# Performance work log

Hardware: AMD Instinct MI355X
Metric: run time of the kernel (lower is better)

The kernel has to match this reference:

```python
import jax, jax.numpy as jnp
import numpy as np

N, E, DIN, DH, R = 50000, 1600000, 128, 128, 3


def setup_inputs() -> dict:
    key = jax.random.key(0)
    ks = jax.random.split(key, 32)
    inp = {}
    inp["x"] = jax.random.normal(ks[0], (N, DIN), jnp.float32)
    inp["h_prev"] = jax.random.normal(ks[1], (N, DH), jnp.float32)
    inp["edge_index"] = jax.random.randint(ks[2], (2, E), 0, N)
    inp["node_role"] = jax.random.randint(ks[3], (N,), 0, R)
    i = 4
    for name, din, has_b in (("xz", DIN, True), ("hz", DH, False), ("xr", DIN, True), ("hr", DH, False), ("xh", DIN, True), ("hh", DH, False)):
        inp[name + "_W"] = jax.random.normal(ks[i], (din, DH), jnp.float32) / np.float32(np.sqrt(din)); i += 1
        inp[name + "_Wg"] = jax.random.normal(ks[i], (R, DH), jnp.float32) * np.float32(0.1); i += 1
        inp[name + "_bg"] = jnp.zeros((R, DH), jnp.float32)
        inp[name + "_S"] = jax.random.normal(ks[i], (R, DH, DH), jnp.float32) / np.float32(np.sqrt(DH)); i += 1
        if has_b:
            inp[name + "_b"] = jnp.zeros((R, DH), jnp.float32)
    return inp


def _role_conv(x, W, Wg, bg, S, b, row, col, node_role):
    # x: [N, din] -> transformed features [N, DH]
    xt = x @ W
    r = node_role[row]                                  # role of source node per edge
    g = jax.nn.sigmoid(Wg[r] + bg[r])                   # [Etot, DH] role gate
    msg = xt[row] * g
    if b is not None:
        msg = msg + b[r]
    n = x.shape[0]
    summed = jax.ops.segment_sum(msg, col, num_segments=n)
    cnt = jax.ops.segment_sum(jnp.ones((row.shape[0],), xt.dtype), col, num_segments=n)
    aggr = summed / jnp.maximum(cnt, 1.0)[:, None]      # scatter_mean (self-loops ensure cnt>=1)
    # per-role self transform: out[i] = xt[i] @ S[role[i]] + aggr[i]
    out = aggr
    for nr in range(R):
        out = out + jnp.where((node_role == nr)[:, None], xt @ S[nr], jnp.float32(0.0))
    return jax.nn.relu(out)


def reference(x, edge_index, h_prev, node_role,
              xz_W, xz_Wg, xz_bg, xz_S, xz_b,
              hz_W, hz_Wg, hz_bg, hz_S,
              xr_W, xr_Wg, xr_bg, xr_S, xr_b,
              hr_W, hr_Wg, hr_bg, hr_S,
              xh_W, xh_Wg, xh_bg, xh_S, xh_b,
              hh_W, hh_Wg, hh_bg, hh_S):
    n = x.shape[0]
    loops = jnp.arange(n, dtype=edge_index.dtype)
    row = jnp.concatenate([edge_index[0], loops])       # add_self_loops appended at end
    col = jnp.concatenate([edge_index[1], loops])

    z = jax.nn.sigmoid(_role_conv(x, xz_W, xz_Wg, xz_bg, xz_S, xz_b, row, col, node_role)
                       + _role_conv(h_prev, hz_W, hz_Wg, hz_bg, hz_S, None, row, col, node_role))
    r = jax.nn.sigmoid(_role_conv(x, xr_W, xr_Wg, xr_bg, xr_S, xr_b, row, col, node_role)
                       + _role_conv(h_prev, hr_W, hr_Wg, hr_bg, hr_S, None, row, col, node_role))
    h_tilde = jnp.tanh(_role_conv(x, xh_W, xh_Wg, xh_bg, xh_S, xh_b, row, col, node_role)
                       + _role_conv(r * h_prev, hh_W, hh_Wg, hh_bg, hh_S, None, row, col, node_role))
    h_new = z * h_prev + (1.0 - z) * h_tilde
    return h_new
```

## Files before the change

### kernel.cpp

```cpp
#include <hip/hip_runtime.h>


typedef __bf16 bf16;
typedef __bf16 bf16x8 __attribute__((ext_vector_type(8)));
typedef float  f32x4  __attribute__((ext_vector_type(4)));
typedef float  f32x2  __attribute__((ext_vector_type(2)));
typedef unsigned char u8;

#define DH 128

__device__ __forceinline__ float sigmoidf_(float x) { return 1.0f / (1.0f + expf(-x)); }

__global__ __launch_bounds__(256) void hist_kernel(const int* __restrict__ ei, const int* __restrict__ role,
                                                   int* __restrict__ cnt3, int* __restrict__ rolecnt,
                                                   int E, int N)
{
  int i = blockIdx.x * 256 + threadIdx.x;
  int lane = threadIdx.x & 63;
  int r = (i < N) ? role[i] : -1;
  #pragma unroll
  for (int rr = 0; rr < 3; ++rr) {
    unsigned long long mask = __ballot(r == rr);
    if (lane == 0 && mask) atomicAdd(&rolecnt[rr], __popcll(mask));
  }
  if (i < E + N) {
    int src, dst;
    if (i < E) { src = ei[i]; dst = ei[E + i]; } else { src = i - E; dst = i - E; }
    int rs = (i < E) ? role[src] : r;
    if (i >= E) rs = role[i - E];
    atomicAdd(&cnt3[dst * 3 + rs], 1);
  }
}

__global__ __launch_bounds__(1024) void scan1_kernel(const int* __restrict__ cnt, int* __restrict__ off,
                                                     int* __restrict__ bsum, int n)
{
  __shared__ int wsum[16];
  int t = threadIdx.x, lane = t & 63, w = t >> 6;
  int idx = blockIdx.x * 1024 + t;
  int v = (idx < n) ? cnt[idx] : 0;
  int s = v;
  #pragma unroll
  for (int d = 1; d < 64; d <<= 1) { int u = __shfl_up(s, d); if (lane >= d) s += u; }
  if (lane == 63) wsum[w] = s;
  __syncthreads();
  if (w == 0 && lane < 16) {
    int ws = wsum[lane];
    #pragma unroll
    for (int d = 1; d < 16; d <<= 1) { int u = __shfl_up(ws, d); if (lane >= d) ws += u; }
    wsum[lane] = ws;
  }
  __syncthreads();
  int inc = ((w > 0) ? wsum[w - 1] : 0) + s;
  if (idx < n) off[idx + 1] = inc;
  if (t == 1023) bsum[blockIdx.x] = inc;
}

__global__ void scan2_kernel(int* __restrict__ bsum, int nb, const int* __restrict__ rolecnt,
                             int* __restrict__ rolefill, int* __restrict__ roleinfo)
{
  int lane = threadIdx.x;
  int carry = 0;
  for (int base = 0; base < nb; base += 64) {
    int v = (base + lane < nb) ? bsum[base + lane] : 0;
    int s = v;
    #pragma unroll
    for (int d = 1; d < 64; d <<= 1) { int u = __shfl_up(s, d); if (lane >= d) s += u; }
    if (base + lane < nb) bsum[base + lane] = carry + s - v;
    carry += __shfl(s, 63);
  }
  if (lane == 0) {
    int c0 = rolecnt[0], c1 = rolecnt[1], c2 = rolecnt[2];
    int s1 = (c0 + 255) & ~255;
    int s2 = s1 + ((c1 + 255) & ~255);
    int mp = s2 + ((c2 + 255) & ~255);
    rolefill[0] = 0; rolefill[1] = s1; rolefill[2] = s2;
    roleinfo[0] = s1; roleinfo[1] = s2;
    roleinfo[2] = c0;      roleinfo[3] = s1 - c0;
    roleinfo[4] = s1 + c1; roleinfo[5] = s2 - s1 - c1;
    roleinfo[6] = s2 + c2; roleinfo[7] = mp - s2 - c2;
  }
}

__global__ __launch_bounds__(1024) void scan3_kernel(int* __restrict__ off, int* __restrict__ fill,
                                                     const int* __restrict__ bsum, int n)
{
  int idx = blockIdx.x * 1024 + threadIdx.x;
  if (idx == 0) { off[0] = 0; fill[0] = 0; }
  if (idx < n) {
    int v = off[idx + 1] + bsum[blockIdx.x];
    off[idx + 1] = v;
    if (idx + 1 < n) fill[idx + 1] = v;
  }
}

__global__ void bucketinit_kernel(const int* __restrict__ off3, int* __restrict__ bucketfill,
                                  int NB, int W, int N)
{
  int b = blockIdx.x * 256 + threadIdx.x;
  if (b < NB) {
    int d = min(b * W, N);
    bucketfill[b] = off3[d * 3];
  }
}

__global__ __launch_bounds__(256) void partition_kernel(
    const int* __restrict__ ei, const int* __restrict__ spos,
    const int* __restrict__ roleinfo, int* __restrict__ bucketfill,
    int2* __restrict__ recs, int E, int N, int shiftB)
{
  __shared__ int lcnt[256], lbase[256];
  const int base = blockIdx.x * 4096;
  const int s1 = roleinfo[0], s2 = roleinfo[1];
  lcnt[threadIdx.x] = 0;
  __syncthreads();
  int myb[16], mybin[16], myt[16];
  #pragma unroll
  for (int k = 0; k < 16; ++k) {
    int i = base + k * 256 + threadIdx.x;
    myb[k] = -1;
    if (i < E + N) {
      int src, dst;
      if (i < E) { src = ei[i]; dst = ei[E + i]; } else { src = i - E; dst = i - E; }
      int t = spos[src];
      int r = (t >= s2) ? 2 : (t >= s1) ? 1 : 0;
      myb[k] = dst >> shiftB;
      mybin[k] = dst * 3 + r;
      myt[k] = t;
      atomicAdd(&lcnt[myb[k]], 1);
    }
  }
  __syncthreads();
  int c = lcnt[threadIdx.x];
  lbase[threadIdx.x] = (c > 0) ? atomicAdd(&bucketfill[threadIdx.x], c) : 0;
  __syncthreads();
  lcnt[threadIdx.x] = 0;
  __syncthreads();
  #pragma unroll
  for (int k = 0; k < 16; ++k) {
    if (myb[k] >= 0) {
      int slot = atomicAdd(&lcnt[myb[k]], 1);
      recs[lbase[myb[k]] + slot] = make_int2(mybin[k], myt[k]);
    }
  }
}

__global__ __launch_bounds__(1024) void binscatter_kernel(
    const int2* __restrict__ recs, const int* __restrict__ off3,
    int* __restrict__ fill3, int* __restrict__ ssrc, int W, int N)
{
  int b = blockIdx.x;
  int d0 = min(b * W, N), d1 = min((b + 1) * W, N);
  int s = off3[d0 * 3], e = off3[d1 * 3];
  for (int i = s + threadIdx.x; i < e; i += 1024) {
    int2 rec = recs[i];
    int pz = atomicAdd(&fill3[rec.x], 1);
    ssrc[pz] = rec.y;
  }
}

__global__ __launch_bounds__(256) void permscatter_kernel(const int* __restrict__ role, int* __restrict__ rolefill,
                                                          int* __restrict__ spos, int* __restrict__ sposinv, int N)
{
  int i = blockIdx.x * 256 + threadIdx.x;
  int lane = threadIdx.x & 63;
  int r = (i < N) ? role[i] : -1;
  #pragma unroll
  for (int rr = 0; rr < 3; ++rr) {
    unsigned long long mask = __ballot(r == rr);
    if (!mask) continue;
    int base = 0;
    if (lane == 0) base = atomicAdd(&rolefill[rr], __popcll(mask));
    base = __shfl(base, 0);
    if (r == rr) {
      int rank = (int)__popcll(mask & ((1ull << lane) - 1ull));
      int pos = base + rank;
      spos[i] = pos;
      sposinv[pos] = i;
    }
  }
}

__global__ __launch_bounds__(256) void zeropad_kernel(const int* __restrict__ roleinfo,
                                                      bf16* __restrict__ Ax, bf16* __restrict__ Ah)
{
  int id = blockIdx.x * 256 + threadIdx.x;
  int a = id / 49152, rem = id % 49152;
  int gp = rem / 16384, r2 = rem % 16384;
  int rr = r2 >> 6, c = r2 & 63;
  int gs = roleinfo[2 + gp * 2], gl = roleinfo[3 + gp * 2];
  if (rr < gl) {
    int row = gs + rr;
    size_t unit = (size_t)(row >> 4) * 1024 + c * 16 + (row & 15);
    bf16x8 z = {};
    ((bf16x8*)(a == 0 ? Ax : Ah))[unit] = z;
  }
}

__global__ __launch_bounds__(256) void prep_xh_kernel(const float* __restrict__ x, const float* __restrict__ h,
                                                      const int* __restrict__ spos, u8* __restrict__ xq8,
                                                      bf16* __restrict__ Ax, bf16* __restrict__ Ah, int N)
{
  int g = blockIdx.x * 256 + threadIdx.x;
  if (g >= N * 32) return;
  int n = g >> 5, j = g & 31;
  int t = spos[n];
  const float* src = (j < 16) ? (x + (size_t)n * 128 + (j << 3))
                              : (h + (size_t)n * 128 + ((j - 16) << 3));
  float4 v0 = ((const float4*)src)[0];
  float4 v1 = ((const float4*)src)[1];
  int lo = __builtin_amdgcn_cvt_pk_fp8_f32(v0.x, v0.y, 0, false);
  lo = __builtin_amdgcn_cvt_pk_fp8_f32(v0.z, v0.w, lo, true);
  int hi = __builtin_amdgcn_cvt_pk_fp8_f32(v1.x, v1.y, 0, false);
  hi = __builtin_amdgcn_cvt_pk_fp8_f32(v1.z, v1.w, hi, true);
  *(int2*)(xq8 + (size_t)t * 256 + j * 8) = make_int2(lo, hi);
  bf16x8 o;
  o[0] = (bf16)v0.x; o[1] = (bf16)v0.y; o[2] = (bf16)v0.z; o[3] = (bf16)v0.w;
  o[4] = (bf16)v1.x; o[5] = (bf16)v1.y; o[6] = (bf16)v1.z; o[7] = (bf16)v1.w;
  size_t unit = (size_t)(t >> 4) * 1024 + (48 + (j & 15)) * 16 + (t & 15);
  ((bf16x8*)(j < 16 ? Ax : Ah))[unit] = o;
}

struct PrepW { const float* W[6]; const float* Wg[6]; const float* bg[6]; };
__global__ __launch_bounds__(256) void prep_wf_kernel(PrepW pw, bf16* __restrict__ Wf)
{
  int idx = blockIdx.x * 256 + threadIdx.x;
  if (idx >= 294912) return;
  int cv = idx / 49152, pos = idx % 49152;
  int ks4q = pos >> 10;
  int col = (pos >> 3) & 127, j = pos & 7;
  int k = (ks4q >> 2) * 32 + (ks4q & 3) * 8 + j;
  int r = k >> 7, kk = k & 127;
  float g = sigmoidf_(pw.Wg[cv][r * 128 + col] + pw.bg[cv][r * 128 + col]);
  Wf[idx] = (bf16)(pw.W[cv][kk * 128 + col] * g);
}

struct PrepP { const float* W[6]; const float* S[6]; };
__global__ __launch_bounds__(128) void prep_pf_kernel(PrepP pp, bf16* __restrict__ Pf)
{
  int b = blockIdx.x;
  int cv = b / 384, rem = b % 384;
  int r = rem >> 7, kp = rem & 127;
  int col = threadIdx.x;
  const float* W = pp.W[cv] + (size_t)kp * 128;
  const float* S = pp.S[cv] + (size_t)r * 16384;
  float sum = 0.f;
  #pragma unroll 4
  for (int j2 = 0; j2 < 128; ++j2) sum += W[j2] * S[j2 * 128 + col];
  size_t o = (size_t)(cv * 3 + r) * 16384 + ((size_t)(kp >> 3) * 128 + col) * 8 + (kp & 7);
  Pf[o] = (bf16)sum;
}

#define ACCUM16(U, d) do { f32x2 f_;                                                   \
  f_ = __builtin_amdgcn_cvt_pk_f32_fp8((d).x, false); U[0]  += f_[0]; U[1]  += f_[1];  \
  f_ = __builtin_amdgcn_cvt_pk_f32_fp8((d).x, true);  U[2]  += f_[0]; U[3]  += f_[1];  \
  f_ = __builtin_amdgcn_cvt_pk_f32_fp8((d).y, false); U[4]  += f_[0]; U[5]  += f_[1];  \
  f_ = __builtin_amdgcn_cvt_pk_f32_fp8((d).y, true);  U[6]  += f_[0]; U[7]  += f_[1];  \
  f_ = __builtin_amdgcn_cvt_pk_f32_fp8((d).z, false); U[8]  += f_[0]; U[9]  += f_[1];  \
  f_ = __builtin_amdgcn_cvt_pk_f32_fp8((d).z, true);  U[10] += f_[0]; U[11] += f_[1];  \
  f_ = __builtin_amdgcn_cvt_pk_f32_fp8((d).w, false); U[12] += f_[0]; U[13] += f_[1];  \
  f_ = __builtin_amdgcn_cvt_pk_f32_fp8((d).w, true);  U[14] += f_[0]; U[15] += f_[1];  \
} while (0)

#define ACCSEL16(d, p) do {                      \
  if ((p) < o1)      { ACCUM16(u0, d); }         \
  else if ((p) < o2) { ACCUM16(u1, d); }         \
  else               { ACCUM16(u2, d); }         \
} while (0)

__global__ __launch_bounds__(512) void gather_xh_kernel(
    const u8* __restrict__ xq8, const int* __restrict__ off3, const int* __restrict__ ssrc,
    const int* __restrict__ sposinv, bf16* __restrict__ Ax, bf16* __restrict__ Ah,
    float4* __restrict__ cntf)
{
  __shared__ alignas(16) bf16 lds[8][768];
  int w = threadIdx.x >> 6, lane = threadIdx.x & 63;
  int t0 = blockIdx.x * 8;
  int t = t0 + w;
  int node = sposinv[t];
  int qt = lane >> 4, ql = lane & 15;

  if (node >= 0) {
    int o0 = __builtin_amdgcn_readfirstlane(off3[node * 3]);
    int o1 = __builtin_amdgcn_readfirstlane(off3[node * 3 + 1]);
    int o2 = __builtin_amdgcn_readfirstlane(off3[node * 3 + 2]);
    int o3 = __builtin_amdgcn_readfirstlane(off3[node * 3 + 3]);
    float inv = 1.0f / (float)(o3 - o0);
    const u8* base = xq8 + ql * 16;

    float u0[16], u1[16], u2[16];
    #pragma unroll
    for (int k = 0; k < 16; ++k) { u0[k] = 0.f; u1[k] = 0.f; u2[k] = 0.f; }

    const int e = o3, emax = o3 - 1;
    for (int i = o0; i < e; i += 16) {
      int p0 = i + qt, p1 = p0 + 4, p2 = p0 + 8, p3 = p0 + 12;
      int t0i = ssrc[min(p0, emax)];
      int t1i = ssrc[min(p1, emax)];
      int t2i = ssrc[min(p2, emax)];
      int t3i = ssrc[min(p3, emax)];
      int4 d0 = make_int4(0, 0, 0, 0), d1 = d0, d2 = d0, d3 = d0;
      if (p0 < e) d0 = *(const int4*)(base + (size_t)t0i * 256);
      if (p1 < e) d1 = *(const int4*)(base + (size_t)t1i * 256);
      if (p2 < e) d2 = *(const int4*)(base + (size_t)t2i * 256);
      if (p3 < e) d3 = *(const int4*)(base + (size_t)t3i * 256);
      ACCSEL16(d0, p0);
      ACCSEL16(d1, p1);
      ACCSEL16(d2, p2);
      ACCSEL16(d3, p3);
    }

    #pragma unroll
    for (int k = 0; k < 16; ++k) {
      u0[k] += __shfl_xor(u0[k], 16); u0[k] += __shfl_xor(u0[k], 32);
      u1[k] += __shfl_xor(u1[k], 16); u1[k] += __shfl_xor(u1[k], 32);
      u2[k] += __shfl_xor(u2[k], 16); u2[k] += __shfl_xor(u2[k], 32);
    }
    if (qt == 0) {
      bf16x8 p0v, p1v;
      int sb0 = (ql < 8) ? (ql * 16) : (384 + (ql - 8) * 16);
      #pragma unroll
      for (int k = 0; k < 8; ++k) { p0v[k] = (bf16)(u0[k] * inv); p1v[k] = (bf16)(u0[8 + k] * inv); }
      *(bf16x8*)&lds[w][sb0] = p0v;
      *(bf16x8*)&lds[w][sb0 + 8] = p1v;
      #pragma unroll
      for (int k = 0; k < 8; ++k) { p0v[k] = (bf16)(u1[k] * inv); p1v[k] = (bf16)(u1[8 + k] * inv); }
      *(bf16x8*)&lds[w][sb0 + 128] = p0v;
      *(bf16x8*)&lds[w][sb0 + 136] = p1v;
      #pragma unroll
      for (int k = 0; k < 8; ++k) { p0v[k] = (bf16)(u2[k] * inv); p1v[k] = (bf16)(u2[8 + k] * inv); }
      *(bf16x8*)&lds[w][sb0 + 256] = p0v;
      *(bf16x8*)&lds[w][sb0 + 264] = p1v;
    }
    if (lane == 0)
      cntf[t] = make_float4((o1 - o0) * inv, (o2 - o1) * inv, (o3 - o2) * inv, (float)(o3 - o0));
  } else {
    if (lane < 48) {
      bf16x8 z = {};
      *(bf16x8*)&lds[w][lane * 16] = z;
      *(bf16x8*)&lds[w][lane * 16 + 8] = z;
    }
    if (lane == 0) cntf[t] = make_float4(0.f, 0.f, 0.f, 0.f);
  }

  __syncthreads();

  int tid = threadIdx.x;
  if (tid < 384) {
    int lc = tid >> 3, row = tid & 7;
    size_t unit = (size_t)(t0 >> 4) * 1024 + lc * 16 + (t0 & 15) + row;
    __builtin_nontemporal_store(*(const bf16x8*)&lds[row][lc * 8], (bf16x8*)Ax + unit);
    __builtin_nontemporal_store(*(const bf16x8*)&lds[row][384 + lc * 8], (bf16x8*)Ah + unit);
  }
}

#define ACCUM8(U, d) do { f32x2 f_;                                                  \
  f_ = __builtin_amdgcn_cvt_pk_f32_fp8((d).x, false); U[0] += f_[0]; U[1] += f_[1];  \
  f_ = __builtin_amdgcn_cvt_pk_f32_fp8((d).x, true);  U[2] += f_[0]; U[3] += f_[1];  \
  f_ = __builtin_amdgcn_cvt_pk_f32_fp8((d).y, false); U[4] += f_[0]; U[5] += f_[1];  \
  f_ = __builtin_amdgcn_cvt_pk_f32_fp8((d).y, true);  U[6] += f_[0]; U[7] += f_[1];  \
} while (0)

#define ACCSEL8(d, p) do {                      \
  if ((p) < o1)      { ACCUM8(v0, d); }         \
  else if ((p) < o2) { ACCUM8(v1, d); }         \
  else               { ACCUM8(v2, d); }         \
} while (0)

__global__ __launch_bounds__(512) void gather_q_kernel(
    const u8* __restrict__ q8, const int* __restrict__ off3, const int* __restrict__ ssrc,
    const int* __restrict__ sposinv, bf16* __restrict__ Aq)
{
  __shared__ alignas(16) bf16 lds[8][384];
  int w = threadIdx.x >> 6, lane = threadIdx.x & 63;
  int t0 = blockIdx.x * 8;
  int t = t0 + w;
  int node = sposinv[t];
  int qt = lane >> 4, ql = lane & 15;

  if (node >= 0) {
    int o0 = __builtin_amdgcn_readfirstlane(off3[node * 3]);
    int o1 = __builtin_amdgcn_readfirstlane(off3[node * 3 + 1]);
    int o2 = __builtin_amdgcn_readfirstlane(off3[node * 3 + 2]);
    int o3 = __builtin_amdgcn_readfirstlane(off3[node * 3 + 3]);
    float inv = 1.0f / (float)(o3 - o0);
    const u8* base = q8 + ql * 8;

    float v0[8], v1[8], v2[8];
    #pragma unroll
    for (int k = 0; k < 8; ++k) { v0[k] = 0.f; v1[k] = 0.f; v2[k] = 0.f; }

    const int e = o3, emax = o3 - 1;
    for (int i = o0; i < e; i += 16) {
      int p0 = i + qt, p1 = p0 + 4, p2 = p0 + 8, p3 = p0 + 12;
      int t0i = ssrc[min(p0, emax)];
      int t1i = ssrc[min(p1, emax)];
      int t2i = ssrc[min(p2, emax)];
      int t3i = ssrc[min(p3, emax)];
      int2 d0 = make_int2(0, 0), d1 = d0, d2 = d0, d3 = d0;
      if (p0 < e) d0 = *(const int2*)(base + (size_t)t0i * 128);
      if (p1 < e) d1 = *(const int2*)(base + (size_t)t1i * 128);
      if (p2 < e) d2 = *(const int2*)(base + (size_t)t2i * 128);
      if (p3 < e) d3 = *(const int2*)(base + (size_t)t3i * 128);
      ACCSEL8(d0, p0);
      ACCSEL8(d1, p1);
      ACCSEL8(d2, p2);
      ACCSEL8(d3, p3);
    }

    #pragma unroll
    for (int k = 0; k < 8; ++k) {
      v0[k] += __shfl_xor(v0[k], 16); v0[k] += __shfl_xor(v0[k], 32);
      v1[k] += __shfl_xor(v1[k], 16); v1[k] += __shfl_xor(v1[k], 32);
      v2[k] += __shfl_xor(v2[k], 16); v2[k] += __shfl_xor(v2[k], 32);
    }
    if (qt == 0) {
      bf16x8 pk;
      #pragma unroll
      for (int k = 0; k < 8; ++k) pk[k] = (bf16)(v0[k] * inv);
      *(bf16x8*)&lds[w][ql * 8] = pk;
      #pragma unroll
      for (int k = 0; k < 8; ++k) pk[k] = (bf16)(v1[k] * inv);
      *(bf16x8*)&lds[w][128 + ql * 8] = pk;
      #pragma unroll
      for (int k = 0; k < 8; ++k) pk[k] = (bf16)(v2[k] * inv);
      *(bf16x8*)&lds[w][256 + ql * 8] = pk;
    }
  } else {
    if (lane < 48) {
      bf16x8 z = {};
      *(bf16x8*)&lds[w][lane * 8] = z;
    }
  }

  __syncthreads();

  int tid = threadIdx.x;
  if (tid < 384) {
    int lc = tid >> 3, row = tid & 7;
    size_t unit = (size_t)(t0 >> 4) * 1024 + lc * 16 + (t0 & 15) + row;
    __builtin_nontemporal_store(*(const bf16x8*)&lds[row][lc * 8], (bf16x8*)Aq + unit);
  }
}

struct GArgs {
  const bf16* Ap[5];
  const bf16* wf[5];
  const bf16* pf[5];
  bf16* out[5];
  const float* bias[5];
};

__global__ __launch_bounds__(256, 3) void gemm_kernel(GArgs ga, const float4* __restrict__ cntf,
                                                      const int* __restrict__ roleinfo)
{
  const int cv = blockIdx.y;
  const bf16* __restrict__ Ap = ga.Ap[cv];
  const bf16* __restrict__ wf = ga.wf[cv];
  const bf16* __restrict__ pf = ga.pf[cv];
  bf16* __restrict__ out = ga.out[cv];
  const float* __restrict__ bias = ga.bias[cv];

  const int w = threadIdx.x >> 6, lane = threadIdx.x & 63;
  const int q = lane >> 4, l = lane & 15;
  const int rb0 = blockIdx.x * 8 + w * 2;
  const int row0 = blockIdx.x * 128;
  const int s1 = roleinfo[0], s2 = roleinfo[1];
  const int role = (row0 >= s2) ? 2 : (row0 >= s1) ? 1 : 0;
  const int laneoff = q * 128 + l;

  f32x4 acc[2][8];
  #pragma unroll
  for (int j = 0; j < 2; ++j)
    #pragma unroll
    for (int ct = 0; ct < 8; ++ct)
      #pragma unroll
      for (int k = 0; k < 4; ++k) acc[j][ct][k] = 0.f;

  const bf16x8* A0 = (const bf16x8*)Ap + (size_t)rb0 * 1024 + lane;
  const bf16x8* WF = (const bf16x8*)wf + laneoff;
  const bf16x8* PF = (const bf16x8*)pf + role * 2048 + laneoff;

  #pragma unroll 2
  for (int ks = 0; ks < 16; ++ks) {
    const bf16x8* bp = (ks < 12) ? (WF + ks * 512) : (PF + (ks - 12) * 512);
    bf16x8 a0 = A0[ks * 64];
    bf16x8 a1 = A0[1024 + ks * 64];
    #pragma unroll
    for (int ct = 0; ct < 8; ++ct) {
      bf16x8 b = bp[ct * 16];
      acc[0][ct] = __builtin_amdgcn_mfma_f32_16x16x32_bf16(a0, b, acc[0][ct], 0, 0, 0);
      acc[1][ct] = __builtin_amdgcn_mfma_f32_16x16x32_bf16(a1, b, acc[1][ct], 0, 0, 0);
    }
  }

  const bool hb = (bias != nullptr);
  #pragma unroll
  for (int j = 0; j < 2; ++j) {
    int rb = rb0 + j;
    float4 cfs[4];
    if (hb) {
      #pragma unroll
      for (int reg = 0; reg < 4; ++reg) cfs[reg] = cntf[rb * 16 + q * 4 + reg];
    }
    #pragma unroll
    for (int ct = 0; ct < 8; ++ct) {
      int col = ct * 16 + l;
      float b0 = 0, b1 = 0, b2 = 0;
      if (hb) { b0 = bias[col]; b1 = bias[128 + col]; b2 = bias[256 + col]; }
      #pragma unroll
      for (int reg = 0; reg < 4; ++reg) {
        int t = rb * 16 + q * 4 + reg;
        float v = acc[j][ct][reg];
        if (hb) v += cfs[reg].x * b0 + cfs[reg].y * b1 + cfs[reg].z * b2;
        out[(size_t)t * 128 + col] = (bf16)fmaxf(v, 0.f);
      }
    }
  }
}

__global__ __launch_bounds__(256) void combine1_kernel(
    const bf16* __restrict__ o0, const bf16* __restrict__ o1,
    const bf16* __restrict__ o2, const bf16* __restrict__ o3,
    const float* __restrict__ h, const int* __restrict__ spos,
    float* __restrict__ zbuf, u8* __restrict__ q8, bf16* __restrict__ Aq, int N)
{
  int g = blockIdx.x * 256 + threadIdx.x;
  if (g >= N * 16) return;
  int n = g >> 4, o = g & 15;
  int t = spos[n];
  size_t tb = (size_t)t * 16 + o;
  bf16x8 a0 = ((const bf16x8*)o0)[tb];
  bf16x8 a1 = ((const bf16x8*)o1)[tb];
  bf16x8 a2 = ((const bf16x8*)o2)[tb];
  bf16x8 a3 = ((const bf16x8*)o3)[tb];
  size_t nb = (size_t)n * 16 + o;
  float4 h0 = ((const float4*)h)[nb * 2];
  float4 h1 = ((const float4*)h)[nb * 2 + 1];
  float hv[8] = {h0.x, h0.y, h0.z, h0.w, h1.x, h1.y, h1.z, h1.w};
  float zv[8], qv[8];
  bf16x8 qb;
  #pragma unroll
  for (int j = 0; j < 8; ++j) {
    zv[j] = sigmoidf_((float)a0[j] + (float)a1[j]);
    qv[j] = sigmoidf_((float)a2[j] + (float)a3[j]) * hv[j];
    qb[j] = (bf16)qv[j];
  }
  ((float4*)zbuf)[nb * 2]     = make_float4(zv[0], zv[1], zv[2], zv[3]);
  ((float4*)zbuf)[nb * 2 + 1] = make_float4(zv[4], zv[5], zv[6], zv[7]);
  int lo = __builtin_amdgcn_cvt_pk_fp8_f32(qv[0], qv[1], 0, false);
  lo = __builtin_amdgcn_cvt_pk_fp8_f32(qv[2], qv[3], lo, true);
  int hi = __builtin_amdgcn_cvt_pk_fp8_f32(qv[4], qv[5], 0, false);
  hi = __builtin_amdgcn_cvt_pk_fp8_f32(qv[6], qv[7], hi, true);
  *(int2*)(q8 + (size_t)t * 128 + o * 8) = make_int2(lo, hi);
  size_t unit = (size_t)(t >> 4) * 1024 + (48 + o) * 16 + (t & 15);
  ((bf16x8*)Aq)[unit] = qb;
}

__global__ __launch_bounds__(256) void combine2_kernel(
    const float* __restrict__ zbuf, const bf16* __restrict__ o4, const bf16* __restrict__ o5,
    const float* __restrict__ h, const int* __restrict__ spos, float* __restrict__ out, int N)
{
  int g = blockIdx.x * 256 + threadIdx.x;
  if (g >= N * 16) return;
  int n = g >> 4, o = g & 15;
  int t = spos[n];
  size_t tb = (size_t)t * 16 + o;
  bf16x8 a = ((const bf16x8*)o4)[tb];
  bf16x8 b = ((const bf16x8*)o5)[tb];
  size_t nb = (size_t)n * 16 + o;
  float4 z0 = ((const float4*)zbuf)[nb * 2];
  float4 z1 = ((const float4*)zbuf)[nb * 2 + 1];
  float4 h0 = ((const float4*)h)[nb * 2];
  float4 h1 = ((const float4*)h)[nb * 2 + 1];
  float zv[8] = {z0.x, z0.y, z0.z, z0.w, z1.x, z1.y, z1.z, z1.w};
  float hv[8] = {h0.x, h0.y, h0.z, h0.w, h1.x, h1.y, h1.z, h1.w};
  float ov[8];
  #pragma unroll
  for (int j = 0; j < 8; ++j)
    ov[j] = zv[j] * hv[j] + (1.f - zv[j]) * tanhf((float)a[j] + (float)b[j]);
  ((float4*)out)[nb * 2]     = make_float4(ov[0], ov[1], ov[2], ov[3]);
  ((float4*)out)[nb * 2 + 1] = make_float4(ov[4], ov[5], ov[6], ov[7]);
}

extern "C" void kernel_launch(void* const* d_in, const int* in_sizes, int n_in,
                              void* d_out, int out_size, void* d_ws, size_t ws_size,
                              hipStream_t stream)
{
  (void)n_in; (void)out_size; (void)ws_size;
  const float* x    = (const float*)d_in[0];
  const float* h    = (const float*)d_in[1];
  const int*   ei   = (const int*)d_in[2];
  const int*   role = (const int*)d_in[3];
  const int N = in_sizes[0] / DH;
  const int E = in_sizes[2] / 2;
  const int Etot = E + N;
  const int rows_pad = ((N + 765) + 255) & ~255;
  const int gx = rows_pad / 128;
  const int n3 = N * 3;
  const int nb3 = (n3 + 1023) / 1024;

  int shiftB = 8;
  while (((N - 1) >> shiftB) >= 256) ++shiftB;
  const int W = 1 << shiftB;
  const int NB = (N + W - 1) >> shiftB;

  static const int Wi[6]  = {4, 9, 13, 18, 22, 27};
  static const int Wgi[6] = {5, 10, 14, 19, 23, 28};
  static const int bgi[6] = {6, 11, 15, 20, 24, 29};
  static const int Si[6]  = {7, 12, 16, 21, 25, 30};

  char* p = (char*)d_ws;
  auto alloc = [&](size_t bytes) -> char* {
    char* r = p;
    p += (bytes + 255) & ~(size_t)255;
    return r;
  };

  bf16* Ax = (bf16*)alloc((size_t)rows_pad * 512 * 2);
  bf16* Ah = (bf16*)alloc((size_t)rows_pad * 512 * 2);
  bf16* Aq = Ax;
  u8* xq8  = (u8*)alloc((size_t)rows_pad * 256);
  u8* q8   = (u8*)alloc((size_t)rows_pad * 128);
  bf16* outs[6];
  for (int c = 0; c < 5; ++c) outs[c] = (bf16*)alloc((size_t)rows_pad * 128 * 2);
  outs[5] = outs[0];
  float* zbuf = (float*)alloc((size_t)N * 128 * 4);
  float4* cntf = (float4*)alloc((size_t)rows_pad * 16);
  bf16* Wf = (bf16*)alloc((size_t)6 * 49152 * 2);
  bf16* Pf = (bf16*)alloc((size_t)18 * 16384 * 2);
  int* cnt3  = (int*)alloc((size_t)n3 * 4);
  int* off3  = (int*)alloc((size_t)(n3 + 1) * 4);
  int* fill3 = (int*)alloc((size_t)n3 * 4);
  int* bsum  = (int*)alloc((size_t)(nb3 + 1) * 4);
  int* ssrc  = (int*)alloc((size_t)Etot * 4);
  int2* recs = (int2*)alloc((size_t)Etot * 8);
  int* spos  = (int*)alloc((size_t)N * 4);
  int* sposinv = (int*)alloc((size_t)rows_pad * 4);
  int* rolecnt  = (int*)alloc(64);
  int* rolefill = (int*)alloc(64);
  int* roleinfo = (int*)alloc(64);
  int* bucketfill = (int*)alloc((size_t)(NB + 1) * 4);

  hipMemsetAsync(cnt3, 0, (size_t)n3 * 4, stream);
  hipMemsetAsync(rolecnt, 0, 16, stream);
  hipMemsetAsync(sposinv, 0xFF, (size_t)rows_pad * 4, stream);

  int egrid = (Etot + 255) / 256;
  int ngrid = (N + 255) / 256;
  hist_kernel<<<egrid, 256, 0, stream>>>(ei, role, cnt3, rolecnt, E, N);
  scan1_kernel<<<nb3, 1024, 0, stream>>>(cnt3, off3, bsum, n3);
  scan2_kernel<<<1, 64, 0, stream>>>(bsum, nb3, rolecnt, rolefill, roleinfo);
  scan3_kernel<<<nb3, 1024, 0, stream>>>(off3, fill3, bsum, n3);
  permscatter_kernel<<<ngrid, 256, 0, stream>>>(role, rolefill, spos, sposinv, N);
  bucketinit_kernel<<<1, 256, 0, stream>>>(off3, bucketfill, NB, W, N);
  partition_kernel<<<(Etot + 4095) / 4096, 256, 0, stream>>>(ei, spos, roleinfo, bucketfill,
                                                             recs, E, N, shiftB);
  binscatter_kernel<<<NB, 1024, 0, stream>>>(recs, off3, fill3, ssrc, W, N);
  zeropad_kernel<<<384, 256, 0, stream>>>(roleinfo, Ax, Ah);

  prep_xh_kernel<<<(N * 32 + 255) / 256, 256, 0, stream>>>(x, h, spos, xq8, Ax, Ah, N);

  PrepW pw;
  for (int c = 0; c < 6; ++c) {
    pw.W[c] = (const float*)d_in[Wi[c]];
    pw.Wg[c] = (const float*)d_in[Wgi[c]];
    pw.bg[c] = (const float*)d_in[bgi[c]];
  }
  prep_wf_kernel<<<1152, 256, 0, stream>>>(pw, Wf);
  PrepP pp;
  for (int c = 0; c < 6; ++c) { pp.W[c] = (const float*)d_in[Wi[c]]; pp.S[c] = (const float*)d_in[Si[c]]; }
  prep_pf_kernel<<<2304, 128, 0, stream>>>(pp, Pf);

  gather_xh_kernel<<<rows_pad / 8, 512, 0, stream>>>(xq8, off3, ssrc, sposinv, Ax, Ah, cntf);

  GArgs g0;
  { int cvs[5] = {0, 2, 4, 1, 3};
    static const int bi2[5] = {8, 17, 26, -1, -1};
    const bf16* Apts[5] = {Ax, Ax, Ax, Ah, Ah};
    for (int k = 0; k < 5; ++k) {
      int c = cvs[k];
      g0.Ap[k] = Apts[k];
      g0.wf[k] = Wf + (size_t)c * 49152;
      g0.pf[k] = Pf + (size_t)c * 3 * 16384;
      g0.out[k] = outs[c];
      g0.bias[k] = (bi2[k] >= 0) ? (const float*)d_in[bi2[k]] : nullptr;
    } }
  gemm_kernel<<<dim3(gx, 5), 256, 0, stream>>>(g0, cntf, roleinfo);

  combine1_kernel<<<(N * 16 + 255) / 256, 256, 0, stream>>>(outs[0], outs[1], outs[2], outs[3],
                                                            h, spos, zbuf, q8, Aq, N);

  gather_q_kernel<<<rows_pad / 8, 512, 0, stream>>>(q8, off3, ssrc, sposinv, Aq);

  GArgs g2 = {};
  g2.Ap[0] = Aq;
  g2.wf[0] = Wf + (size_t)5 * 49152;
  g2.pf[0] = Pf + (size_t)5 * 3 * 16384;
  g2.out[0] = outs[5];
  g2.bias[0] = nullptr;
  gemm_kernel<<<dim3(gx, 1), 256, 0, stream>>>(g2, cntf, roleinfo);

  combine2_kernel<<<(N * 16 + 255) / 256, 256, 0, stream>>>(zbuf, outs[4], outs[5], h, spos,
                                                            (float*)d_out, N);
}
```

Measured before the change: 682.3 us.

## Replace global fine histogram and scans with coarse bucket histogram plus local scans

Removes the per-(dst,role) global atomic histogram over all edges and the three-pass global scan. Instead it builds a coarse per-bucket histogram in shared memory, scans 256 buckets in one block, and computes the fine offsets inside binscatter through a shared-memory histogram and scan per bucket. This cuts global atomics and memory traffic in the CSR build. The trade-off is extra shared-memory atomics and block-level scans inside binscatter, and it relies on each bucket holding at most 1024 local (dst,role) slots.

```diff
diff --git a/kernel.cpp b/kernel.cpp
--- a/kernel.cpp
+++ b/kernel.cpp
@@ -11,9 +11,8 @@
 
 __device__ __forceinline__ float sigmoidf_(float x) { return 1.0f / (1.0f + expf(-x)); }
 
-__global__ __launch_bounds__(256) void hist_kernel(const int* __restrict__ ei, const int* __restrict__ role,
-                                                   int* __restrict__ cnt3, int* __restrict__ rolecnt,
-                                                   int E, int N)
+__global__ __launch_bounds__(256) void rolecnt_kernel(const int* __restrict__ role,
+                                                      int* __restrict__ rolecnt, int N)
 {
   int i = blockIdx.x * 256 + threadIdx.x;
   int lane = threadIdx.x & 63;
@@ -23,53 +22,12 @@
     unsigned long long mask = __ballot(r == rr);
     if (lane == 0 && mask) atomicAdd(&rolecnt[rr], __popcll(mask));
   }
-  if (i < E + N) {
-    int src, dst;
-    if (i < E) { src = ei[i]; dst = ei[E + i]; } else { src = i - E; dst = i - E; }
-    int rs = (i < E) ? role[src] : r;
-    if (i >= E) rs = role[i - E];
-    atomicAdd(&cnt3[dst * 3 + rs], 1);
-  }
-}
-
-__global__ __launch_bounds__(1024) void scan1_kernel(const int* __restrict__ cnt, int* __restrict__ off,
-                                                     int* __restrict__ bsum, int n)
-{
-  __shared__ int wsum[16];
-  int t = threadIdx.x, lane = t & 63, w = t >> 6;
-  int idx = blockIdx.x * 1024 + t;
-  int v = (idx < n) ? cnt[idx] : 0;
-  int s = v;
-  #pragma unroll
-  for (int d = 1; d < 64; d <<= 1) { int u = __shfl_up(s, d); if (lane >= d) s += u; }
-  if (lane == 63) wsum[w] = s;
-  __syncthreads();
-  if (w == 0 && lane < 16) {
-    int ws = wsum[lane];
-    #pragma unroll
-    for (int d = 1; d < 16; d <<= 1) { int u = __shfl_up(ws, d); if (lane >= d) ws += u; }
-    wsum[lane] = ws;
-  }
-  __syncthreads();
-  int inc = ((w > 0) ? wsum[w - 1] : 0) + s;
-  if (idx < n) off[idx + 1] = inc;
-  if (t == 1023) bsum[blockIdx.x] = inc;
-}
-
-__global__ void scan2_kernel(int* __restrict__ bsum, int nb, const int* __restrict__ rolecnt,
-                             int* __restrict__ rolefill, int* __restrict__ roleinfo)
-{
-  int lane = threadIdx.x;
-  int carry = 0;
-  for (int base = 0; base < nb; base += 64) {
-    int v = (base + lane < nb) ? bsum[base + lane] : 0;
-    int s = v;
-    #pragma unroll
-    for (int d = 1; d < 64; d <<= 1) { int u = __shfl_up(s, d); if (lane >= d) s += u; }
-    if (base + lane < nb) bsum[base + lane] = carry + s - v;
-    carry += __shfl(s, 63);
-  }
-  if (lane == 0) {
+}
+
+__global__ void roleinfo_kernel(const int* __restrict__ rolecnt,
+                                int* __restrict__ rolefill, int* __restrict__ roleinfo)
+{
+  if (threadIdx.x == 0) {
     int c0 = rolecnt[0], c1 = rolecnt[1], c2 = rolecnt[2];
     int s1 = (c0 + 255) & ~255;
     int s2 = s1 + ((c1 + 255) & ~255);
@@ -82,26 +40,66 @@
   }
 }
 
-__global__ __launch_bounds__(1024) void scan3_kernel(int* __restrict__ off, int* __restrict__ fill,
-                                                     const int* __restrict__ bsum, int n)
-{
-  int idx = blockIdx.x * 1024 + threadIdx.x;
-  if (idx == 0) { off[0] = 0; fill[0] = 0; }
-  if (idx < n) {
-    int v = off[idx + 1] + bsum[blockIdx.x];
-    off[idx + 1] = v;
-    if (idx + 1 < n) fill[idx + 1] = v;
-  }
-}
-
-__global__ void bucketinit_kernel(const int* __restrict__ off3, int* __restrict__ bucketfill,
-                                  int NB, int W, int N)
-{
-  int b = blockIdx.x * 256 + threadIdx.x;
-  if (b < NB) {
-    int d = min(b * W, N);
-    bucketfill[b] = off3[d * 3];
-  }
+__global__ __launch_bounds__(256) void permscatter_kernel(const int* __restrict__ role, int* __restrict__ rolefill,
+                                                          int* __restrict__ spos, int* __restrict__ sposinv, int N)
+{
+  int i = blockIdx.x * 256 + threadIdx.x;
+  int lane = threadIdx.x & 63;
+  int r = (i < N) ? role[i] : -1;
+  #pragma unroll
+  for (int rr = 0; rr < 3; ++rr) {
+    unsigned long long mask = __ballot(r == rr);
+    if (!mask) continue;
+    int base = 0;
+    if (lane == 0) base = atomicAdd(&rolefill[rr], __popcll(mask));
+    base = __shfl(base, 0);
+    if (r == rr) {
+      int rank = (int)__popcll(mask & ((1ull << lane) - 1ull));
+      int pos = base + rank;
+      spos[i] = pos;
+      sposinv[pos] = i;
+    }
+  }
+}
+
+__global__ __launch_bounds__(256) void coarsehist_kernel(const int* __restrict__ ei,
+                                                         int* __restrict__ bucketcnt,
+                                                         int E, int N, int shiftB)
+{
+  __shared__ int lc[256];
+  lc[threadIdx.x] = 0;
+  __syncthreads();
+  const int base = blockIdx.x * 4096;
+  #pragma unroll
+  for (int k = 0; k < 16; ++k) {
+    int i = base + k * 256 + threadIdx.x;
+    if (i < E + N) {
+      int dst = (i < E) ? ei[E + i] : i - E;
+      atomicAdd(&lc[dst >> shiftB], 1);
+    }
+  }
+  __syncthreads();
+  int c = lc[threadIdx.x];
+  if (c > 0) atomicAdd(&bucketcnt[threadIdx.x], c);
+}
+
+__global__ __launch_bounds__(256) void bucketscan_kernel(const int* __restrict__ bucketcnt,
+                                                         int* __restrict__ bucketbase,
+                                                         int* __restrict__ bucketfill, int NB)
+{
+  __shared__ int lh[256];
+  int tid = threadIdx.x;
+  lh[tid] = (tid < NB) ? bucketcnt[tid] : 0;
+  __syncthreads();
+  for (int d = 1; d < 256; d <<= 1) {
+    int v = (tid >= d) ? lh[tid - d] : 0;
+    __syncthreads();
+    lh[tid] += v;
+    __syncthreads();
+  }
+  int excl = (tid > 0) ? lh[tid - 1] : 0;
+  if (tid < NB) { bucketbase[tid] = excl; bucketfill[tid] = excl; }
+  if (tid == 0) bucketbase[NB] = lh[255];
 }
 
 __global__ __launch_bounds__(256) void partition_kernel(
@@ -146,38 +144,38 @@
 }
 
 __global__ __launch_bounds__(1024) void binscatter_kernel(
-    const int2* __restrict__ recs, const int* __restrict__ off3,
-    int* __restrict__ fill3, int* __restrict__ ssrc, int W, int N)
-{
+    const int2* __restrict__ recs, const int* __restrict__ bucketbase,
+    int* __restrict__ off3, int* __restrict__ ssrc, int W, int N, int NB)
+{
+  __shared__ int lh[1024];
   int b = blockIdx.x;
+  int tid = threadIdx.x;
   int d0 = min(b * W, N), d1 = min((b + 1) * W, N);
-  int s = off3[d0 * 3], e = off3[d1 * 3];
-  for (int i = s + threadIdx.x; i < e; i += 1024) {
+  int nloc = (d1 - d0) * 3;
+  int s = bucketbase[b], e = bucketbase[b + 1];
+  int lb0 = d0 * 3;
+
+  lh[tid] = 0;
+  __syncthreads();
+  for (int i = s + tid; i < e; i += 1024)
+    atomicAdd(&lh[recs[i].x - lb0], 1);
+  __syncthreads();
+  for (int d = 1; d < 1024; d <<= 1) {
+    int v = (tid >= d) ? lh[tid - d] : 0;
+    __syncthreads();
+    lh[tid] += v;
+    __syncthreads();
+  }
+  if (tid < nloc) off3[lb0 + tid] = s + ((tid > 0) ? lh[tid - 1] : 0);
+  if (b == NB - 1 && tid == 0) off3[N * 3] = e;
+  int excl = (tid > 0) ? lh[tid - 1] : 0;
+  __syncthreads();
+  lh[tid] = excl;
+  __syncthreads();
+  for (int i = s + tid; i < e; i += 1024) {
     int2 rec = recs[i];
-    int pz = atomicAdd(&fill3[rec.x], 1);
-    ssrc[pz] = rec.y;
-  }
-}
-
-__global__ __launch_bounds__(256) void permscatter_kernel(const int* __restrict__ role, int* __restrict__ rolefill,
-                                                          int* __restrict__ spos, int* __restrict__ sposinv, int N)
-{
-  int i = blockIdx.x * 256 + threadIdx.x;
-  int lane = threadIdx.x & 63;
-  int r = (i < N) ? role[i] : -1;
-  #pragma unroll
-  for (int rr = 0; rr < 3; ++rr) {
-    unsigned long long mask = __ballot(r == rr);
-    if (!mask) continue;
-    int base = 0;
-    if (lane == 0) base = atomicAdd(&rolefill[rr], __popcll(mask));
-    base = __shfl(base, 0);
-    if (r == rr) {
-      int rank = (int)__popcll(mask & ((1ull << lane) - 1ull));
-      int pos = base + rank;
-      spos[i] = pos;
-      sposinv[pos] = i;
-    }
+    int slot = atomicAdd(&lh[rec.x - lb0], 1);
+    ssrc[s + slot] = rec.y;
   }
 }
 
@@ -598,7 +596,6 @@
   const int rows_pad = ((N + 765) + 255) & ~255;
   const int gx = rows_pad / 128;
   const int n3 = N * 3;
-  const int nb3 = (n3 + 1023) / 1024;
 
   int shiftB = 8;
   while (((N - 1) >> shiftB) >= 256) ++shiftB;
@@ -629,10 +626,7 @@
   float4* cntf = (float4*)alloc((size_t)rows_pad * 16);
   bf16* Wf = (bf16*)alloc((size_t)6 * 49152 * 2);
   bf16* Pf = (bf16*)alloc((size_t)18 * 16384 * 2);
-  int* cnt3  = (int*)alloc((size_t)n3 * 4);
   int* off3  = (int*)alloc((size_t)(n3 + 1) * 4);
-  int* fill3 = (int*)alloc((size_t)n3 * 4);
-  int* bsum  = (int*)alloc((size_t)(nb3 + 1) * 4);
   int* ssrc  = (int*)alloc((size_t)Etot * 4);
   int2* recs = (int2*)alloc((size_t)Etot * 8);
   int* spos  = (int*)alloc((size_t)N * 4);
@@ -640,23 +634,24 @@
   int* rolecnt  = (int*)alloc(64);
   int* rolefill = (int*)alloc(64);
   int* roleinfo = (int*)alloc(64);
-  int* bucketfill = (int*)alloc((size_t)(NB + 1) * 4);
-
-  hipMemsetAsync(cnt3, 0, (size_t)n3 * 4, stream);
+  int* bucketcnt  = (int*)alloc(257 * 4);
+  int* bucketbase = (int*)alloc(258 * 4);
+  int* bucketfill = (int*)alloc(257 * 4);
+
   hipMemsetAsync(rolecnt, 0, 16, stream);
+  hipMemsetAsync(bucketcnt, 0, 257 * 4, stream);
   hipMemsetAsync(sposinv, 0xFF, (size_t)rows_pad * 4, stream);
 
-  int egrid = (Etot + 255) / 256;
+  int egrid4k = (Etot + 4095) / 4096;
   int ngrid = (N + 255) / 256;
-  hist_kernel<<<egrid, 256, 0, stream>>>(ei, role, cnt3, rolecnt, E, N);
-  scan1_kernel<<<nb3, 1024, 0, stream>>>(cnt3, off3, bsum, n3);
-  scan2_kernel<<<1, 64, 0, stream>>>(bsum, nb3, rolecnt, rolefill, roleinfo);
-  scan3_kernel<<<nb3, 1024, 0, stream>>>(off3, fill3, bsum, n3);
+  rolecnt_kernel<<<ngrid, 256, 0, stream>>>(role, rolecnt, N);
+  roleinfo_kernel<<<1, 64, 0, stream>>>(rolecnt, rolefill, roleinfo);
   permscatter_kernel<<<ngrid, 256, 0, stream>>>(role, rolefill, spos, sposinv, N);
-  bucketinit_kernel<<<1, 256, 0, stream>>>(off3, bucketfill, NB, W, N);
-  partition_kernel<<<(Etot + 4095) / 4096, 256, 0, stream>>>(ei, spos, roleinfo, bucketfill,
-                                                             recs, E, N, shiftB);
-  binscatter_kernel<<<NB, 1024, 0, stream>>>(recs, off3, fill3, ssrc, W, N);
+  coarsehist_kernel<<<egrid4k, 256, 0, stream>>>(ei, bucketcnt, E, N, shiftB);
+  bucketscan_kernel<<<1, 256, 0, stream>>>(bucketcnt, bucketbase, bucketfill, NB);
+  partition_kernel<<<egrid4k, 256, 0, stream>>>(ei, spos, roleinfo, bucketfill,
+                                                recs, E, N, shiftB);
+  binscatter_kernel<<<NB, 1024, 0, stream>>>(recs, bucketbase, off3, ssrc, W, N, NB);
   zeropad_kernel<<<384, 256, 0, stream>>>(roleinfo, Ax, Ah);
 
   prep_xh_kernel<<<(N * 32 + 255) / 256, 256, 0, stream>>>(x, h, spos, xq8, Ax, Ah, N);
```

New measurement: 611.3 us. 1.12x faster.
